# Kernel optimization log

Measured on AMD Instinct MI355X. Metric: run time of the kernel, lower is better.

The kernel has to match this reference:

```python
import jax, jax.numpy as jnp
import numpy as np

N_POS, D_MODEL, D_SAE, TOP_K = 2, 1024, 32768, 32


def setup_inputs() -> dict:
    key = jax.random.key(0)
    k_x, k_we, k_wd = jax.random.split(key, 3)
    x = jax.random.normal(k_x, (4096, N_POS, D_MODEL), dtype=jnp.float32)
    W_enc = jax.random.normal(k_we, (N_POS, D_MODEL, D_SAE), dtype=jnp.float32) * (1.0 / D_MODEL ** 0.5)
    W_dec = jax.random.normal(k_wd, (D_SAE, N_POS, D_MODEL), dtype=jnp.float32) * (1.0 / D_SAE ** 0.5)
    b_enc = jnp.zeros((D_SAE,), dtype=jnp.float32)
    b_dec = jnp.zeros((N_POS, D_MODEL), dtype=jnp.float32)
    return {"x": x, "W_enc": W_enc, "W_dec": W_dec, "b_enc": b_enc, "b_dec": b_dec}


def reference(x, W_enc, W_dec, b_enc, b_dec):
    # Encode: per-position einsum then shared bias -> (batch, d_sae)
    pre_act = jnp.einsum('btd,tds->bs', x, W_enc) + b_enc
    top_vals, top_idx = jax.lax.top_k(pre_act, TOP_K)  # (b, k)
    batch = pre_act.shape[0]
    rows = jnp.arange(batch)[:, None]  # (b, 1) broadcast against (b, k)
    z = jnp.zeros_like(pre_act).at[rows, top_idx].set(jax.nn.relu(top_vals))
    # Decode: dense contraction over d_sae -> (batch, n_positions, d_model)
    x_hat = jnp.einsum('bs,std->btd', z, W_dec) + b_dec
    return x_hat
```

## Files before the change

### kernel.cpp

```cpp
#include <hip/hip_runtime.h>
#include <cstdint>
#include <cstddef>

typedef unsigned short u16;
typedef unsigned long long u64;
typedef __attribute__((ext_vector_type(8))) short short8;
typedef __attribute__((ext_vector_type(4))) float f32x4;

constexpr int K_DIM = 2048;
constexpr int S_DIM = 32768;
constexpr int TOPK  = 32;
constexpr int CAP   = 256;
#define EPS      0.07f
#define THR_EMIT 3.7f
#define HIST_LO  3.5f

__device__ __forceinline__ u16 f2bf(float f) {
    unsigned u = __float_as_uint(f);
    return (u16)((u + 0x7FFFu + ((u >> 16) & 1u)) >> 16);
}
__device__ __forceinline__ float bf2f(u16 h) {
    return __uint_as_float(((unsigned)h) << 16);
}
__device__ __forceinline__ unsigned key_map(float f) {
    unsigned u = __float_as_uint(f);
    return (u & 0x80000000u) ? ~u : (u | 0x80000000u);
}
__device__ __forceinline__ float key_unmap(unsigned k) {
    unsigned u = (k & 0x80000000u) ? (k ^ 0x80000000u) : ~k;
    return __uint_as_float(u);
}

__global__ __launch_bounds__(256) void init_kernel(int* __restrict__ flag, int M)
{
    int i = blockIdx.x * 256 + threadIdx.x;
    if (i < M) flag[i] = 0;
}

__global__ __launch_bounds__(256) void conv_x_kernel(
    const float* __restrict__ x, u16* __restrict__ hi, int n4)
{
    int i = blockIdx.x * 256 + threadIdx.x;
    if (i >= n4) return;
    float4 v = ((const float4*)x)[i];
    ushort4 h;
    h.x = f2bf(v.x); h.y = f2bf(v.y); h.z = f2bf(v.z); h.w = f2bf(v.w);
    ((ushort4*)hi)[i] = h;
}

__global__ __launch_bounds__(256) void conv_wt_kernel(
    const float* __restrict__ W, float* __restrict__ WT, u16* __restrict__ Wh)
{
    __shared__ float tile[64][65];
    const int t  = threadIdx.x;
    const int s0 = blockIdx.x * 64;
    const int k0 = blockIdx.y * 64;
#pragma unroll
    for (int i = 0; i < 4; ++i) {
        int kl = (t >> 4) + i * 16;
        int sc = (t & 15) * 4;
        float4 v = *(const float4*)&W[(size_t)(k0 + kl) * S_DIM + s0 + sc];
        tile[kl][sc] = v.x; tile[kl][sc + 1] = v.y;
        tile[kl][sc + 2] = v.z; tile[kl][sc + 3] = v.w;
    }
    __syncthreads();
    const int klc = (t & 7) * 8;
#pragma unroll
    for (int i = 0; i < 2; ++i) {
        int sl = (t >> 3) + i * 32;
        float f[8];
        short8 h8;
#pragma unroll
        for (int j = 0; j < 8; ++j) {
            f[j] = tile[klc + j][sl];
            h8[j] = (short)f2bf(f[j]);
        }
        size_t o = (size_t)(s0 + sl) * K_DIM + k0 + klc;
        *(float4*)&WT[o]     = make_float4(f[0], f[1], f[2], f[3]);
        *(float4*)&WT[o + 4] = make_float4(f[4], f[5], f[6], f[7]);
        *(short8*)&Wh[o] = h8;
    }
}

__device__ __forceinline__ void gl16(const u16* g, u16* s) {
    __builtin_amdgcn_global_load_lds(
        (const __attribute__((address_space(1))) unsigned int*)g,
        (__attribute__((address_space(3))) unsigned int*)s,
        16, 0, 0);
}

#define LGKM0  do { asm volatile("s_waitcnt lgkmcnt(0)" ::: "memory"); \
                    __builtin_amdgcn_sched_barrier(0); } while (0)
#define VMW(n) asm volatile("s_waitcnt vmcnt(" #n ")" ::: "memory")
#define BAR    do { __builtin_amdgcn_s_barrier(); \
                    __builtin_amdgcn_sched_barrier(0); } while (0)

__global__ __launch_bounds__(512, 2) void gemm_mfma_kernel(
    const u16* __restrict__ A, const u16* __restrict__ B,
    const float* __restrict__ bias, u16* __restrict__ Cb)
{
    __shared__ alignas(16) u16 sMem[65536];
    u16* sA0 = sMem;
    u16* sB0 = sMem + 32768;

    const int t = threadIdx.x;
    const int lane = t & 63;
    const int w = t >> 6;
    const int wm = w >> 2, wn = w & 3;

    const int nwg = gridDim.x;
    const int q = nwg >> 3;
    const int bid = blockIdx.x;
    const int wg = (bid & 7) * q + (bid >> 3);
    const int bm = wg >> 7;
    const int bn = wg & 127;

    const u16* Ab = A + (size_t)bm * 256 * K_DIM;
    const u16* Bb = B + (size_t)bn * 256 * K_DIM;

    const int w2  = w * 2;
    const int lr3 = lane >> 3;
    const int csw = ((lane & 7) ^ lr3) * 8;

    const int rl = lane & 15, kq = lane >> 4;
    const int swz = rl & 7;
    const int ac0 = (kq ^ swz) * 8;
    const int ac1 = ((4 + kq) ^ swz) * 8;
    const int arow = (wm * 16 + rl) * 64;
    const int brow = (wn * 16 + rl) * 64;

    f32x4 acc[8][4];
#pragma unroll
    for (int m = 0; m < 8; ++m)
#pragma unroll
        for (int n = 0; n < 4; ++n) acc[m][n] = (f32x4){0.f, 0.f, 0.f, 0.f};

    auto stA = [&](int half, int j, int kt, int buf) {
        const u16* src = Ab + (size_t)(half * 128 + (w2 + j) * 8 + lr3) * K_DIM
                            + kt * 64 + csw;
        gl16(src, sA0 + buf * 16384 + half * 8192 + (w2 + j) * 512);
    };
    auto stB = [&](int half, int j, int kt, int buf) {
        const u16* src = Bb + (size_t)(half * 128 + (w2 + j) * 8 + lr3) * K_DIM
                            + kt * 64 + csw;
        gl16(src, sB0 + buf * 16384 + half * 8192 + (w2 + j) * 512);
    };

    stB(0, 0, 0, 0); stB(0, 1, 0, 0);
    stA(0, 0, 0, 0); stA(0, 1, 0, 0);
    stB(1, 0, 0, 0); stB(1, 1, 0, 0);
    stA(1, 0, 0, 0); stA(1, 1, 0, 0);
    stB(0, 0, 1, 1); stB(0, 1, 1, 1);
    stA(0, 0, 1, 1); stA(0, 1, 1, 1);
    stB(1, 0, 1, 1); stB(1, 1, 1, 1);
    VMW(6);
    BAR;

    short8 af[4][2], bf[4][2];

#pragma unroll
    for (int n = 0; n < 2; ++n) {
        bf[n][0] = *(const short8*)&sB0[brow + n * 4096 + ac0];
        bf[n][1] = *(const short8*)&sB0[brow + n * 4096 + ac1];
    }

#pragma unroll 1
    for (int it = 0; it < 16; ++it) {
        const bool lastIt = (it == 15);
#pragma unroll
        for (int h = 0; h < 2; ++h) {
            const int b  = h;
            const int tA = 2 * it + 1 + h;
            const int tB = 2 * it + 2 + h;

#pragma unroll
            for (int m = 0; m < 4; ++m) {
                af[m][0] = *(const short8*)&sA0[b * 16384 + arow + m * 2048 + ac0];
                af[m][1] = *(const short8*)&sA0[b * 16384 + arow + m * 2048 + ac1];
            }
            if (tA < 32) { stA(1, 0, tA, b ^ 1); stA(1, 1, tA, b ^ 1); }
            __builtin_amdgcn_s_barrier();
            LGKM0;
            __builtin_amdgcn_s_setprio(1);
#pragma unroll
            for (int m = 0; m < 4; ++m)
#pragma unroll
                for (int n = 0; n < 2; ++n)
#pragma unroll
                    for (int kk = 0; kk < 2; ++kk)
                        acc[m][n] = __builtin_amdgcn_mfma_f32_16x16x32_bf16(
                            af[m][kk], bf[n][kk], acc[m][n], 0, 0, 0);
            __builtin_amdgcn_s_setprio(0);
            BAR;

#pragma unroll
            for (int n = 2; n < 4; ++n) {
                bf[n][0] = *(const short8*)&sB0[b * 16384 + brow + n * 4096 + ac0];
                bf[n][1] = *(const short8*)&sB0[b * 16384 + brow + n * 4096 + ac1];
            }
            if (tB < 32) { stB(0, 0, tB, b); stB(0, 1, tB, b); }
            __builtin_amdgcn_s_barrier();
            LGKM0;
            __builtin_amdgcn_s_setprio(1);
#pragma unroll
            for (int m = 0; m < 4; ++m)
#pragma unroll
                for (int n = 2; n < 4; ++n)
#pragma unroll
                    for (int kk = 0; kk < 2; ++kk)
                        acc[m][n] = __builtin_amdgcn_mfma_f32_16x16x32_bf16(
                            af[m][kk], bf[n][kk], acc[m][n], 0, 0, 0);
            __builtin_amdgcn_s_setprio(0);
            BAR;

#pragma unroll
            for (int m = 0; m < 4; ++m) {
                af[m][0] = *(const short8*)&sA0[b * 16384 + arow + (m + 4) * 2048 + ac0];
                af[m][1] = *(const short8*)&sA0[b * 16384 + arow + (m + 4) * 2048 + ac1];
            }
            if (tB < 32) { stA(0, 0, tB, b); stA(0, 1, tB, b); }
            __builtin_amdgcn_s_barrier();
            LGKM0;
            __builtin_amdgcn_s_setprio(1);
#pragma unroll
            for (int m = 0; m < 4; ++m)
#pragma unroll
                for (int n = 2; n < 4; ++n)
#pragma unroll
                    for (int kk = 0; kk < 2; ++kk)
                        acc[m + 4][n] = __builtin_amdgcn_mfma_f32_16x16x32_bf16(
                            af[m][kk], bf[n][kk], acc[m + 4][n], 0, 0, 0);
            __builtin_amdgcn_s_setprio(0);
            BAR;

            if (tB < 32) { stB(1, 0, tB, b); stB(1, 1, tB, b); }
            __builtin_amdgcn_s_barrier();
            __builtin_amdgcn_s_setprio(1);
#pragma unroll
            for (int m = 0; m < 4; ++m)
#pragma unroll
                for (int n = 0; n < 2; ++n)
#pragma unroll
                    for (int kk = 0; kk < 2; ++kk)
                        acc[m + 4][n] = __builtin_amdgcn_mfma_f32_16x16x32_bf16(
                            af[m][kk], bf[n][kk], acc[m + 4][n], 0, 0, 0);
            __builtin_amdgcn_s_setprio(0);
            if (lastIt && h == 0) { VMW(0); } else { VMW(6); }
            if (!(lastIt && h == 1)) {
#pragma unroll
                for (int n = 0; n < 2; ++n) {
                    bf[n][0] = *(const short8*)&sB0[(b ^ 1) * 16384 + brow + n * 4096 + ac0];
                    bf[n][1] = *(const short8*)&sB0[(b ^ 1) * 16384 + brow + n * 4096 + ac1];
                }
            }
            BAR;
        }
    }

    {
        const int colL = wn * 16 + rl;
        const int rowL = wm * 16 + kq * 4;
        float bv[4];
#pragma unroll
        for (int n = 0; n < 4; ++n) bv[n] = bias[bn * 256 + colL + n * 64];
#pragma unroll
        for (int m = 0; m < 8; ++m)
#pragma unroll
            for (int n = 0; n < 4; ++n)
#pragma unroll
                for (int rr = 0; rr < 4; ++rr)
                    sMem[(rowL + m * 32 + rr) * 256 + colL + n * 64] =
                        f2bf(acc[m][n][rr] + bv[n]);
        __syncthreads();

        const int rr2 = t >> 5;
        const int c16 = t & 31;
        const size_t growB = (size_t)bm * 256;
#pragma unroll
        for (int r = 0; r < 16; ++r) {
            const int lrow = r * 16 + rr2;
            short8 v = *(const short8*)&sMem[lrow * 256 + c16 * 8];
            *(short8*)&Cb[(growB + lrow) * S_DIM + bn * 256 + c16 * 8] = v;
        }
    }
}

__global__ __launch_bounds__(256) void screen_kernel(
    const u16* __restrict__ pre, u64* __restrict__ emit,
    int* __restrict__ ccnt, float* __restrict__ thrv,
    int* __restrict__ flag, int row0)
{
    __shared__ unsigned hist[64];
    __shared__ int cnt;

    const int t = threadIdx.x;
    const int row = blockIdx.x;
    const int grow = row0 + row;
    const u16* prow = pre + (size_t)row * S_DIM;

    if (t < 64) hist[t] = 0;
    if (t == 0) cnt = 0;
    __syncthreads();

    u64* erow = emit + (size_t)grow * CAP;
    for (int i = t * 8; i < S_DIM; i += 2048) {
        short8 v8 = *(const short8*)&prow[i];
#pragma unroll
        for (int j = 0; j < 8; ++j) {
            float v = bf2f((u16)v8[j]);
            if (v >= HIST_LO) {
                int b = (int)((v - HIST_LO) * 25.0f);
                if (b > 63) b = 63;
                atomicAdd(&hist[b], 1u);
                if (v >= THR_EMIT) {
                    int p = atomicAdd(&cnt, 1);
                    if (p < CAP)
                        erow[p] = ((u64)key_map(v) << 32) | (unsigned)(i + j);
                }
            }
        }
    }
    __syncthreads();

    if (t == 0) {
        unsigned acc = 0;
        int b = -1;
        for (int j = 63; j >= 0; --j) {
            acc += hist[j];
            if (acc >= (unsigned)TOPK) { b = j; break; }
        }
        float thr = HIST_LO + 0.04f * b - 2.0f * EPS - 1e-4f;
        if (b < 0 || cnt > CAP || thr < THR_EMIT) {
            flag[grow] = 1;
            thr = THR_EMIT;
        }
        thrv[grow] = thr;
        ccnt[grow] = (cnt < CAP) ? cnt : CAP;
    }
}

__global__ __launch_bounds__(256) void rescore_kernel(
    const float* __restrict__ x, const float* __restrict__ WT,
    const float* __restrict__ benc, const u64* __restrict__ emit,
    const int* __restrict__ ccnt, const float* __restrict__ thrv,
    float* __restrict__ resc, int row0)
{
    const int row = row0 + blockIdx.x;
    const int t = threadIdx.x;
    const int w = t >> 6, l = t & 63;
    const int cnt = ccnt[row];
    const float thr = thrv[row];

    __shared__ float xs[K_DIM];
    const float* xr = x + (size_t)row * K_DIM;
    for (int i = t * 4; i < K_DIM; i += 1024)
        *(float4*)&xs[i] = *(const float4*)&xr[i];
    __syncthreads();

    for (int c = w; c < cnt; c += 4) {
        const u64 pk = emit[(size_t)row * CAP + c];
        const float approx = key_unmap((unsigned)(pk >> 32));
        if (approx < thr) {
            if (l == 0) resc[(size_t)row * CAP + c] = -3e38f;
            continue;
        }
        const int s = (int)(pk & 0xFFFFFFFFu);
        const float* wc = WT + (size_t)s * K_DIM;
        float acc = 0.f;
#pragma unroll
        for (int j = 0; j < 32; ++j)
            acc = fmaf(xs[l + 64 * j], wc[l + 64 * j], acc);
#pragma unroll
        for (int d = 1; d < 64; d <<= 1) acc += __shfl_xor(acc, d);
        if (l == 0) resc[(size_t)row * CAP + c] = acc + benc[s];
    }
}

__global__ __launch_bounds__(64) void select_kernel(
    const float* __restrict__ resc, const u64* __restrict__ emit,
    const int* __restrict__ ccnt, const float* __restrict__ thrv,
    float* __restrict__ tv, int* __restrict__ ti, int* __restrict__ flag,
    int row0)
{
    const int row = row0 + blockIdx.x;
    const int l = threadIdx.x;
    const int cnt = ccnt[row];

    float v[4] = {0.f, 0.f, 0.f, 0.f};
    int   s[4] = {-1, -1, -1, -1};
    u64   p[4] = {0, 0, 0, 0};
#pragma unroll
    for (int j = 0; j < 4; ++j) {
        int c = l + j * 64;
        if (c < cnt) {
            s[j] = (int)(emit[(size_t)row * CAP + c] & 0xFFFFFFFFu);
            v[j] = resc[(size_t)row * CAP + c];
            p[j] = ((u64)key_map(v[j]) << 32) | (unsigned)(~s[j]);
        }
    }

    float* tvr = tv + (size_t)row * TOPK;
    int*   tir = ti + (size_t)row * TOPK;
    float v32f = -3e38f;
#pragma unroll 1
    for (int r = 0; r < TOPK; ++r) {
        u64 m = p[0];
        if (p[1] > m) m = p[1];
        if (p[2] > m) m = p[2];
        if (p[3] > m) m = p[3];
#pragma unroll
        for (int d = 1; d < 64; d <<= 1) {
            u64 o = __shfl_xor(m, d);
            if (o > m) m = o;
        }
        if (r == TOPK - 1) v32f = key_unmap((unsigned)(m >> 32));
        if (p[0] == m)      { tvr[r] = v[0]; tir[r] = s[0] < 0 ? 0 : s[0]; p[0] = 0; }
        else if (p[1] == m) { tvr[r] = v[1]; tir[r] = s[1] < 0 ? 0 : s[1]; p[1] = 0; }
        else if (p[2] == m) { tvr[r] = v[2]; tir[r] = s[2] < 0 ? 0 : s[2]; p[2] = 0; }
        else if (p[3] == m) { tvr[r] = v[3]; tir[r] = s[3] < 0 ? 0 : s[3]; p[3] = 0; }
    }
    if (l == 0) {
        if (v32f < thrv[row] + EPS) flag[row] = 1;
    }
}

__global__ __launch_bounds__(256) void fb_screen_kernel(
    const u16* __restrict__ pre, u64* __restrict__ emit,
    int* __restrict__ ccnt, const int* __restrict__ flag, int row0)
{
    const int grow = row0 + blockIdx.x;
    if (!flag[grow]) return;

    __shared__ unsigned hist[2048];
    __shared__ unsigned partial[256];
    __shared__ unsigned sh_tk;
    __shared__ int cnt;

    const int t = threadIdx.x;
    const u16* prow = pre + (size_t)blockIdx.x * S_DIM;

    for (int i = t; i < 2048; i += 256) hist[i] = 0;
    if (t == 0) cnt = 0;
    __syncthreads();

    for (int i = t * 8; i < S_DIM; i += 2048) {
        short8 v8 = *(const short8*)&prow[i];
#pragma unroll
        for (int j = 0; j < 8; ++j) {
            unsigned k = key_map(bf2f((u16)v8[j]));
            if (k >= 0xC0000000u) atomicAdd(&hist[(k >> 19) - 6144], 1u);
        }
    }
    __syncthreads();

    unsigned ps = 0;
#pragma unroll
    for (int j = 0; j < 8; ++j) ps += hist[t * 8 + j];
    partial[t] = ps;
    __syncthreads();

    if (t == 0) {
        unsigned acc = 0;
        int seg = -1;
        for (int s = 255; s >= 0; --s) {
            if (acc + partial[s] >= (unsigned)TOPK) { seg = s; break; }
            acc += partial[s];
        }
        int bucket = 6144;
        if (seg >= 0) {
            for (int b = seg * 8 + 7; b >= seg * 8; --b) {
                acc += hist[b];
                if (acc >= (unsigned)TOPK) { bucket = 6144 + b; break; }
            }
        }
        float lo = key_unmap(((unsigned)bucket) << 19) - 2.0f * EPS;
        sh_tk = key_map(lo);
    }
    __syncthreads();

    const unsigned TK = sh_tk;
    u64* erow = emit + (size_t)grow * CAP;
    for (int i = t * 8; i < S_DIM; i += 2048) {
        short8 v8 = *(const short8*)&prow[i];
#pragma unroll
        for (int j = 0; j < 8; ++j) {
            unsigned k = key_map(bf2f((u16)v8[j]));
            if (k >= TK) {
                int p = atomicAdd(&cnt, 1);
                if (p < CAP) erow[p] = ((u64)k << 32) | (unsigned)(i + j);
            }
        }
    }
    __syncthreads();
    if (t == 0) ccnt[grow] = (cnt < CAP) ? cnt : CAP;
}

__global__ __launch_bounds__(256) void fb_rescore_kernel(
    const float* __restrict__ x, const float* __restrict__ WT,
    const float* __restrict__ benc, const u64* __restrict__ emit,
    const int* __restrict__ ccnt, float* __restrict__ resc,
    const int* __restrict__ flag, int row0)
{
    const int row = row0 + blockIdx.x;
    if (!flag[row]) return;
    const int t = threadIdx.x;
    const int w = t >> 6, l = t & 63;
    const int cnt = ccnt[row];

    __shared__ float xs[K_DIM];
    const float* xr = x + (size_t)row * K_DIM;
    for (int i = t * 4; i < K_DIM; i += 1024)
        *(float4*)&xs[i] = *(const float4*)&xr[i];
    __syncthreads();

    for (int c = w; c < cnt; c += 4) {
        const int s = (int)(emit[(size_t)row * CAP + c] & 0xFFFFFFFFu);
        const float* wc = WT + (size_t)s * K_DIM;
        float acc = 0.f;
#pragma unroll
        for (int j = 0; j < 32; ++j)
            acc = fmaf(xs[l + 64 * j], wc[l + 64 * j], acc);
#pragma unroll
        for (int d = 1; d < 64; d <<= 1) acc += __shfl_xor(acc, d);
        if (l == 0) resc[(size_t)row * CAP + c] = acc + benc[s];
    }
}

__global__ __launch_bounds__(64) void fb_select_kernel(
    const float* __restrict__ resc, const u64* __restrict__ emit,
    const int* __restrict__ ccnt, float* __restrict__ tv,
    int* __restrict__ ti, const int* __restrict__ flag, int row0)
{
    const int row = row0 + blockIdx.x;
    if (!flag[row]) return;
    const int l = threadIdx.x;
    const int cnt = ccnt[row];

    float v[4] = {0.f, 0.f, 0.f, 0.f};
    int   s[4] = {-1, -1, -1, -1};
    u64   p[4] = {0, 0, 0, 0};
#pragma unroll
    for (int j = 0; j < 4; ++j) {
        int c = l + j * 64;
        if (c < cnt) {
            s[j] = (int)(emit[(size_t)row * CAP + c] & 0xFFFFFFFFu);
            v[j] = resc[(size_t)row * CAP + c];
            p[j] = ((u64)key_map(v[j]) << 32) | (unsigned)(~s[j]);
        }
    }

    float* tvr = tv + (size_t)row * TOPK;
    int*   tir = ti + (size_t)row * TOPK;
#pragma unroll 1
    for (int r = 0; r < TOPK; ++r) {
        u64 m = p[0];
        if (p[1] > m) m = p[1];
        if (p[2] > m) m = p[2];
        if (p[3] > m) m = p[3];
#pragma unroll
        for (int d = 1; d < 64; d <<= 1) {
            u64 o = __shfl_xor(m, d);
            if (o > m) m = o;
        }
        if (p[0] == m)      { tvr[r] = v[0]; tir[r] = s[0] < 0 ? 0 : s[0]; p[0] = 0; }
        else if (p[1] == m) { tvr[r] = v[1]; tir[r] = s[1] < 0 ? 0 : s[1]; p[1] = 0; }
        else if (p[2] == m) { tvr[r] = v[2]; tir[r] = s[2] < 0 ? 0 : s[2]; p[2] = 0; }
        else if (p[3] == m) { tvr[r] = v[3]; tir[r] = s[3] < 0 ? 0 : s[3]; p[3] = 0; }
    }
}

__global__ __launch_bounds__(256) void decode_kernel(
    const float* __restrict__ tval, const int* __restrict__ tidx,
    const float* __restrict__ Wd, const float* __restrict__ bdec,
    float* __restrict__ out, int row0)
{
    const int row = row0 + blockIdx.x;
    const int t = threadIdx.x;
    __shared__ float sv[TOPK];
    __shared__ int   si[TOPK];
    if (t < TOPK) {
        sv[t] = fmaxf(tval[(size_t)row * TOPK + t], 0.f);
        si[t] = tidx[(size_t)row * TOPK + t];
    }
    __syncthreads();

    const int c0 = t * 4;
    float4 acc0 = *(const float4*)(bdec + c0);
    float4 acc1 = *(const float4*)(bdec + 1024 + c0);
#pragma unroll 4
    for (int i = 0; i < TOPK; ++i) {
        const float z = sv[i];
        if (z > 0.f) {
            const float* wr = Wd + (size_t)si[i] * K_DIM;
            float4 w0 = *(const float4*)(wr + c0);
            float4 w1 = *(const float4*)(wr + 1024 + c0);
            acc0.x = fmaf(z, w0.x, acc0.x); acc0.y = fmaf(z, w0.y, acc0.y);
            acc0.z = fmaf(z, w0.z, acc0.z); acc0.w = fmaf(z, w0.w, acc0.w);
            acc1.x = fmaf(z, w1.x, acc1.x); acc1.y = fmaf(z, w1.y, acc1.y);
            acc1.z = fmaf(z, w1.z, acc1.z); acc1.w = fmaf(z, w1.w, acc1.w);
        }
    }
    float* op = out + (size_t)row * K_DIM;
    *(float4*)(op + c0) = acc0;
    *(float4*)(op + 1024 + c0) = acc1;
}

extern "C" void kernel_launch(void* const* d_in, const int* in_sizes, int n_in,
                              void* d_out, int out_size, void* d_ws, size_t ws_size,
                              hipStream_t stream)
{
    const float* x     = (const float*)d_in[0];
    const float* W_enc = (const float*)d_in[1];
    const float* W_dec = (const float*)d_in[2];
    const float* b_enc = (const float*)d_in[3];
    const float* b_dec = (const float*)d_in[4];
    float* out = (float*)d_out;

    const int M = in_sizes[0] / K_DIM;

    char* wsb = (char*)d_ws;
    size_t o = 0;
    float*    tv   = (float*)(wsb + o);    o += (size_t)M * TOPK * 4;
    int*      ti   = (int*)(wsb + o);      o += (size_t)M * TOPK * 4;
    u64*      emit = (u64*)(wsb + o);      o += (size_t)M * CAP * 8;
    int*      ccnt = (int*)(wsb + o);      o += (size_t)M * 4;
    float*    thrv = (float*)(wsb + o);    o += (size_t)M * 4;
    int*      flag = (int*)(wsb + o);      o += (size_t)M * 4;
    float*    resc = (float*)(wsb + o);    o += (size_t)M * CAP * 4;
    u16*      Xh   = (u16*)(wsb + o);      o += (size_t)M * K_DIM * 2;
    u16*      Wh   = (u16*)(wsb + o);      o += (size_t)S_DIM * K_DIM * 2;
    float*    WT   = (float*)(wsb + o);    o += (size_t)S_DIM * K_DIM * 4;
    u16*      pre  = (u16*)(wsb + o);

    size_t cap = (ws_size > o) ? (ws_size - o) : 0;
    long cap_rows = (long)(cap / ((size_t)S_DIM * 2));
    int chunk = (int)((cap_rows / 256) * 256);
    if (chunk <= 0) chunk = 256;
    if (chunk > M) chunk = M;

    init_kernel<<<(M + 255) / 256, 256, 0, stream>>>(flag, M);
    const int n4 = M * K_DIM / 4;
    conv_x_kernel<<<(n4 + 255) / 256, 256, 0, stream>>>(x, Xh, n4);
    conv_wt_kernel<<<dim3(S_DIM / 64, K_DIM / 64), 256, 0, stream>>>(W_enc, WT, Wh);

    for (int r0 = 0; r0 < M; r0 += chunk) {
        const int rows = (M - r0 < chunk) ? (M - r0) : chunk;
        const int nbm = rows / 256;
        gemm_mfma_kernel<<<nbm * 128, 512, 0, stream>>>(
            Xh + (size_t)r0 * K_DIM, Wh, b_enc, pre);
        screen_kernel<<<rows, 256, 0, stream>>>(pre, emit, ccnt, thrv, flag, r0);
        rescore_kernel<<<rows, 256, 0, stream>>>(x, WT, b_enc, emit, ccnt, thrv, resc, r0);
        select_kernel<<<rows, 64, 0, stream>>>(resc, emit, ccnt, thrv, tv, ti, flag, r0);
        fb_screen_kernel<<<rows, 256, 0, stream>>>(pre, emit, ccnt, flag, r0);
        fb_rescore_kernel<<<rows, 256, 0, stream>>>(x, WT, b_enc, emit, ccnt, resc, flag, r0);
        fb_select_kernel<<<rows, 64, 0, stream>>>(resc, emit, ccnt, tv, ti, flag, r0);
        decode_kernel<<<rows, 256, 0, stream>>>(tv, ti, W_dec, b_dec, out, r0);
    }
}
```

Before: 1.084 ms.

## Fuse screen/rescore/select/decode into one per-row kernel and swizzle GEMM epilogue LDS

Merges the screen, rescore, select and decode kernels into a single per-row kernel that keeps candidates, rescored values and top-k results in shared memory. The fallback path is merged the same way and overwrites the output for flagged rows. This removes several launches and the global-memory round-trips for emit, resc, tv and ti, and drops the flag init kernel. Separately, the GEMM epilogue's shared-memory tile gets an XOR swizzle to cut bank conflicts. Per-block LDS use grows, which may lower occupancy in the fused kernels.

```diff
diff --git a/kernel.cpp b/kernel.cpp
--- a/kernel.cpp
+++ b/kernel.cpp
@@ -29,12 +29,6 @@
 __device__ __forceinline__ float key_unmap(unsigned k) {
     unsigned u = (k & 0x80000000u) ? (k ^ 0x80000000u) : ~k;
     return __uint_as_float(u);
-}
-
-__global__ __launch_bounds__(256) void init_kernel(int* __restrict__ flag, int M)
-{
-    int i = blockIdx.x * 256 + threadIdx.x;
-    if (i < M) flag[i] = 0;
 }
 
 __global__ __launch_bounds__(256) void conv_x_kernel(
@@ -268,9 +262,13 @@
 #pragma unroll
             for (int n = 0; n < 4; ++n)
 #pragma unroll
-                for (int rr = 0; rr < 4; ++rr)
-                    sMem[(rowL + m * 32 + rr) * 256 + colL + n * 64] =
+                for (int rr = 0; rr < 4; ++rr) {
+                    const int row = rowL + m * 32 + rr;
+                    const int col = colL + n * 64;
+                    const int chs = (col >> 3) ^ (((row >> 2) & 3) << 1);
+                    sMem[row * 256 + (chs << 3) + (col & 7)] =
                         f2bf(acc[m][n][rr] + bv[n]);
+                }
         __syncthreads();
 
         const int rr2 = t >> 5;
@@ -279,19 +277,28 @@
 #pragma unroll
         for (int r = 0; r < 16; ++r) {
             const int lrow = r * 16 + rr2;
-            short8 v = *(const short8*)&sMem[lrow * 256 + c16 * 8];
+            const int chr = c16 ^ (((lrow >> 2) & 3) << 1);
+            short8 v = *(const short8*)&sMem[lrow * 256 + (chr << 3)];
             *(short8*)&Cb[(growB + lrow) * S_DIM + bn * 256 + c16 * 8] = v;
         }
     }
 }
 
-__global__ __launch_bounds__(256) void screen_kernel(
-    const u16* __restrict__ pre, u64* __restrict__ emit,
-    int* __restrict__ ccnt, float* __restrict__ thrv,
-    int* __restrict__ flag, int row0)
+__global__ __launch_bounds__(256) void fused_kernel(
+    const u16* __restrict__ pre, const float* __restrict__ x,
+    const float* __restrict__ WT, const float* __restrict__ benc,
+    const float* __restrict__ Wd, const float* __restrict__ bdec,
+    float* __restrict__ out, int* __restrict__ flag, int row0)
 {
     __shared__ unsigned hist[64];
     __shared__ int cnt;
+    __shared__ float sh_thr;
+    __shared__ int sh_bad;
+    __shared__ u64 emitL[CAP];
+    __shared__ float rescL[CAP];
+    __shared__ float xs[K_DIM];
+    __shared__ float tvL[TOPK];
+    __shared__ int   tiL[TOPK];
 
     const int t = threadIdx.x;
     const int row = blockIdx.x;
@@ -299,10 +306,13 @@
     const u16* prow = pre + (size_t)row * S_DIM;
 
     if (t < 64) hist[t] = 0;
-    if (t == 0) cnt = 0;
-    __syncthreads();
-
-    u64* erow = emit + (size_t)grow * CAP;
+    if (t == 0) { cnt = 0; sh_bad = 0; }
+    __syncthreads();
+
+    const float* xr = x + (size_t)grow * K_DIM;
+    for (int i = t * 4; i < K_DIM; i += 1024)
+        *(float4*)&xs[i] = *(const float4*)&xr[i];
+
     for (int i = t * 8; i < S_DIM; i += 2048) {
         short8 v8 = *(const short8*)&prow[i];
 #pragma unroll
@@ -315,7 +325,7 @@
                 if (v >= THR_EMIT) {
                     int p = atomicAdd(&cnt, 1);
                     if (p < CAP)
-                        erow[p] = ((u64)key_map(v) << 32) | (unsigned)(i + j);
+                        emitL[p] = ((u64)key_map(v) << 32) | (unsigned)(i + j);
                 }
             }
         }
@@ -331,37 +341,22 @@
         }
         float thr = HIST_LO + 0.04f * b - 2.0f * EPS - 1e-4f;
         if (b < 0 || cnt > CAP || thr < THR_EMIT) {
-            flag[grow] = 1;
+            sh_bad = 1;
             thr = THR_EMIT;
         }
-        thrv[grow] = thr;
-        ccnt[grow] = (cnt < CAP) ? cnt : CAP;
-    }
-}
-
-__global__ __launch_bounds__(256) void rescore_kernel(
-    const float* __restrict__ x, const float* __restrict__ WT,
-    const float* __restrict__ benc, const u64* __restrict__ emit,
-    const int* __restrict__ ccnt, const float* __restrict__ thrv,
-    float* __restrict__ resc, int row0)
-{
-    const int row = row0 + blockIdx.x;
-    const int t = threadIdx.x;
-    const int w = t >> 6, l = t & 63;
-    const int cnt = ccnt[row];
-    const float thr = thrv[row];
-
-    __shared__ float xs[K_DIM];
-    const float* xr = x + (size_t)row * K_DIM;
-    for (int i = t * 4; i < K_DIM; i += 1024)
-        *(float4*)&xs[i] = *(const float4*)&xr[i];
-    __syncthreads();
-
-    for (int c = w; c < cnt; c += 4) {
-        const u64 pk = emit[(size_t)row * CAP + c];
+        sh_thr = thr;
+    }
+    __syncthreads();
+
+    const int cntc = (cnt < CAP) ? cnt : CAP;
+    const float thr = sh_thr;
+    const int wv = t >> 6, l = t & 63;
+
+    for (int c = wv; c < cntc; c += 4) {
+        const u64 pk = emitL[c];
         const float approx = key_unmap((unsigned)(pk >> 32));
         if (approx < thr) {
-            if (l == 0) resc[(size_t)row * CAP + c] = -3e38f;
+            if (l == 0) rescL[c] = -3e38f;
             continue;
         }
         const int s = (int)(pk & 0xFFFFFFFFu);
@@ -372,76 +367,97 @@
             acc = fmaf(xs[l + 64 * j], wc[l + 64 * j], acc);
 #pragma unroll
         for (int d = 1; d < 64; d <<= 1) acc += __shfl_xor(acc, d);
-        if (l == 0) resc[(size_t)row * CAP + c] = acc + benc[s];
-    }
-}
-
-__global__ __launch_bounds__(64) void select_kernel(
-    const float* __restrict__ resc, const u64* __restrict__ emit,
-    const int* __restrict__ ccnt, const float* __restrict__ thrv,
-    float* __restrict__ tv, int* __restrict__ ti, int* __restrict__ flag,
-    int row0)
+        if (l == 0) rescL[c] = acc + benc[s];
+    }
+    __syncthreads();
+
+    if (t < 64) {
+        float v[4] = {0.f, 0.f, 0.f, 0.f};
+        int   s[4] = {-1, -1, -1, -1};
+        u64   p[4] = {0, 0, 0, 0};
+#pragma unroll
+        for (int j = 0; j < 4; ++j) {
+            int c = l + j * 64;
+            if (c < cntc) {
+                s[j] = (int)(emitL[c] & 0xFFFFFFFFu);
+                v[j] = rescL[c];
+                p[j] = ((u64)key_map(v[j]) << 32) | (unsigned)(~s[j]);
+            }
+        }
+        float v32f = -3e38f;
+#pragma unroll 1
+        for (int r = 0; r < TOPK; ++r) {
+            u64 m = p[0];
+            if (p[1] > m) m = p[1];
+            if (p[2] > m) m = p[2];
+            if (p[3] > m) m = p[3];
+#pragma unroll
+            for (int d = 1; d < 64; d <<= 1) {
+                u64 o = __shfl_xor(m, d);
+                if (o > m) m = o;
+            }
+            if (r == TOPK - 1) v32f = key_unmap((unsigned)(m >> 32));
+            if (p[0] == m)      { tvL[r] = v[0]; tiL[r] = s[0] < 0 ? 0 : s[0]; p[0] = 0; }
+            else if (p[1] == m) { tvL[r] = v[1]; tiL[r] = s[1] < 0 ? 0 : s[1]; p[1] = 0; }
+            else if (p[2] == m) { tvL[r] = v[2]; tiL[r] = s[2] < 0 ? 0 : s[2]; p[2] = 0; }
+            else if (p[3] == m) { tvL[r] = v[3]; tiL[r] = s[3] < 0 ? 0 : s[3]; p[3] = 0; }
+        }
+        if (l == 0)
+            flag[grow] = (sh_bad || v32f < thr + EPS) ? 1 : 0;
+    }
+    __syncthreads();
+
+    const int c0 = t * 4;
+    float4 acc0 = *(const float4*)(bdec + c0);
+    float4 acc1 = *(const float4*)(bdec + 1024 + c0);
+#pragma unroll 4
+    for (int i = 0; i < TOPK; ++i) {
+        const float z = fmaxf(tvL[i], 0.f);
+        if (z > 0.f) {
+            const float* wr = Wd + (size_t)tiL[i] * K_DIM;
+            float4 w0 = *(const float4*)(wr + c0);
+            float4 w1 = *(const float4*)(wr + 1024 + c0);
+            acc0.x = fmaf(z, w0.x, acc0.x); acc0.y = fmaf(z, w0.y, acc0.y);
+            acc0.z = fmaf(z, w0.z, acc0.z); acc0.w = fmaf(z, w0.w, acc0.w);
+            acc1.x = fmaf(z, w1.x, acc1.x); acc1.y = fmaf(z, w1.y, acc1.y);
+            acc1.z = fmaf(z, w1.z, acc1.z); acc1.w = fmaf(z, w1.w, acc1.w);
+        }
+    }
+    float* op = out + (size_t)grow * K_DIM;
+    *(float4*)(op + c0) = acc0;
+    *(float4*)(op + 1024 + c0) = acc1;
+}
+
+__global__ __launch_bounds__(256) void fb_kernel(
+    const u16* __restrict__ pre, const float* __restrict__ x,
+    const float* __restrict__ WT, const float* __restrict__ benc,
+    const float* __restrict__ Wd, const float* __restrict__ bdec,
+    float* __restrict__ out, const int* __restrict__ flag, int row0)
 {
-    const int row = row0 + blockIdx.x;
-    const int l = threadIdx.x;
-    const int cnt = ccnt[row];
-
-    float v[4] = {0.f, 0.f, 0.f, 0.f};
-    int   s[4] = {-1, -1, -1, -1};
-    u64   p[4] = {0, 0, 0, 0};
-#pragma unroll
-    for (int j = 0; j < 4; ++j) {
-        int c = l + j * 64;
-        if (c < cnt) {
-            s[j] = (int)(emit[(size_t)row * CAP + c] & 0xFFFFFFFFu);
-            v[j] = resc[(size_t)row * CAP + c];
-            p[j] = ((u64)key_map(v[j]) << 32) | (unsigned)(~s[j]);
-        }
-    }
-
-    float* tvr = tv + (size_t)row * TOPK;
-    int*   tir = ti + (size_t)row * TOPK;
-    float v32f = -3e38f;
-#pragma unroll 1
-    for (int r = 0; r < TOPK; ++r) {
-        u64 m = p[0];
-        if (p[1] > m) m = p[1];
-        if (p[2] > m) m = p[2];
-        if (p[3] > m) m = p[3];
-#pragma unroll
-        for (int d = 1; d < 64; d <<= 1) {
-            u64 o = __shfl_xor(m, d);
-            if (o > m) m = o;
-        }
-        if (r == TOPK - 1) v32f = key_unmap((unsigned)(m >> 32));
-        if (p[0] == m)      { tvr[r] = v[0]; tir[r] = s[0] < 0 ? 0 : s[0]; p[0] = 0; }
-        else if (p[1] == m) { tvr[r] = v[1]; tir[r] = s[1] < 0 ? 0 : s[1]; p[1] = 0; }
-        else if (p[2] == m) { tvr[r] = v[2]; tir[r] = s[2] < 0 ? 0 : s[2]; p[2] = 0; }
-        else if (p[3] == m) { tvr[r] = v[3]; tir[r] = s[3] < 0 ? 0 : s[3]; p[3] = 0; }
-    }
-    if (l == 0) {
-        if (v32f < thrv[row] + EPS) flag[row] = 1;
-    }
-}
-
-__global__ __launch_bounds__(256) void fb_screen_kernel(
-    const u16* __restrict__ pre, u64* __restrict__ emit,
-    int* __restrict__ ccnt, const int* __restrict__ flag, int row0)
-{
-    const int grow = row0 + blockIdx.x;
+    const int row = blockIdx.x;
+    const int grow = row0 + row;
     if (!flag[grow]) return;
 
     __shared__ unsigned hist[2048];
     __shared__ unsigned partial[256];
     __shared__ unsigned sh_tk;
     __shared__ int cnt;
+    __shared__ u64 emitL[CAP];
+    __shared__ float rescL[CAP];
+    __shared__ float xs[K_DIM];
+    __shared__ float tvL[TOPK];
+    __shared__ int   tiL[TOPK];
 
     const int t = threadIdx.x;
-    const u16* prow = pre + (size_t)blockIdx.x * S_DIM;
+    const u16* prow = pre + (size_t)row * S_DIM;
 
     for (int i = t; i < 2048; i += 256) hist[i] = 0;
     if (t == 0) cnt = 0;
     __syncthreads();
+
+    const float* xr = x + (size_t)grow * K_DIM;
+    for (int i = t * 4; i < K_DIM; i += 1024)
+        *(float4*)&xs[i] = *(const float4*)&xr[i];
 
     for (int i = t * 8; i < S_DIM; i += 2048) {
         short8 v8 = *(const short8*)&prow[i];
@@ -479,7 +495,6 @@
     __syncthreads();
 
     const unsigned TK = sh_tk;
-    u64* erow = emit + (size_t)grow * CAP;
     for (int i = t * 8; i < S_DIM; i += 2048) {
         short8 v8 = *(const short8*)&prow[i];
 #pragma unroll
@@ -487,34 +502,17 @@
             unsigned k = key_map(bf2f((u16)v8[j]));
             if (k >= TK) {
                 int p = atomicAdd(&cnt, 1);
-                if (p < CAP) erow[p] = ((u64)k << 32) | (unsigned)(i + j);
-            }
-        }
-    }
-    __syncthreads();
-    if (t == 0) ccnt[grow] = (cnt < CAP) ? cnt : CAP;
-}
-
-__global__ __launch_bounds__(256) void fb_rescore_kernel(
-    const float* __restrict__ x, const float* __restrict__ WT,
-    const float* __restrict__ benc, const u64* __restrict__ emit,
-    const int* __restrict__ ccnt, float* __restrict__ resc,
-    const int* __restrict__ flag, int row0)
-{
-    const int row = row0 + blockIdx.x;
-    if (!flag[row]) return;
-    const int t = threadIdx.x;
-    const int w = t >> 6, l = t & 63;
-    const int cnt = ccnt[row];
-
-    __shared__ float xs[K_DIM];
-    const float* xr = x + (size_t)row * K_DIM;
-    for (int i = t * 4; i < K_DIM; i += 1024)
-        *(float4*)&xs[i] = *(const float4*)&xr[i];
-    __syncthreads();
-
-    for (int c = w; c < cnt; c += 4) {
-        const int s = (int)(emit[(size_t)row * CAP + c] & 0xFFFFFFFFu);
+                if (p < CAP) emitL[p] = ((u64)k << 32) | (unsigned)(i + j);
+            }
+        }
+    }
+    __syncthreads();
+
+    const int cntc = (cnt < CAP) ? cnt : CAP;
+    const int wv = t >> 6, l = t & 63;
+
+    for (int c = wv; c < cntc; c += 4) {
+        const int s = (int)(emitL[c] & 0xFFFFFFFFu);
         const float* wc = WT + (size_t)s * K_DIM;
         float acc = 0.f;
 #pragma unroll
@@ -522,65 +520,39 @@
             acc = fmaf(xs[l + 64 * j], wc[l + 64 * j], acc);
 #pragma unroll
         for (int d = 1; d < 64; d <<= 1) acc += __shfl_xor(acc, d);
-        if (l == 0) resc[(size_t)row * CAP + c] = acc + benc[s];
-    }
-}
-
-__global__ __launch_bounds__(64) void fb_select_kernel(
-    const float* __restrict__ resc, const u64* __restrict__ emit,
-    const int* __restrict__ ccnt, float* __restrict__ tv,
-    int* __restrict__ ti, const int* __restrict__ flag, int row0)
-{
-    const int row = row0 + blockIdx.x;
-    if (!flag[row]) return;
-    const int l = threadIdx.x;
-    const int cnt = ccnt[row];
-
-    float v[4] = {0.f, 0.f, 0.f, 0.f};
-    int   s[4] = {-1, -1, -1, -1};
-    u64   p[4] = {0, 0, 0, 0};
-#pragma unroll
-    for (int j = 0; j < 4; ++j) {
-        int c = l + j * 64;
-        if (c < cnt) {
-            s[j] = (int)(emit[(size_t)row * CAP + c] & 0xFFFFFFFFu);
-            v[j] = resc[(size_t)row * CAP + c];
-            p[j] = ((u64)key_map(v[j]) << 32) | (unsigned)(~s[j]);
-        }
-    }
-
-    float* tvr = tv + (size_t)row * TOPK;
-    int*   tir = ti + (size_t)row * TOPK;
+        if (l == 0) rescL[c] = acc + benc[s];
+    }
+    __syncthreads();
+
+    if (t < 64) {
+        float v[4] = {0.f, 0.f, 0.f, 0.f};
+        int   s[4] = {-1, -1, -1, -1};
+        u64   p[4] = {0, 0, 0, 0};
+#pragma unroll
+        for (int j = 0; j < 4; ++j) {
+            int c = l + j * 64;
+            if (c < cntc) {
+                s[j] = (int)(emitL[c] & 0xFFFFFFFFu);
+                v[j] = rescL[c];
+                p[j] = ((u64)key_map(v[j]) << 32) | (unsigned)(~s[j]);
+            }
+        }
 #pragma unroll 1
-    for (int r = 0; r < TOPK; ++r) {
-        u64 m = p[0];
-        if (p[1] > m) m = p[1];
-        if (p[2] > m) m = p[2];
-        if (p[3] > m) m = p[3];
-#pragma unroll
-        for (int d = 1; d < 64; d <<= 1) {
-            u64 o = __shfl_xor(m, d);
-            if (o > m) m = o;
-        }
-        if (p[0] == m)      { tvr[r] = v[0]; tir[r] = s[0] < 0 ? 0 : s[0]; p[0] = 0; }
-        else if (p[1] == m) { tvr[r] = v[1]; tir[r] = s[1] < 0 ? 0 : s[1]; p[1] = 0; }
-        else if (p[2] == m) { tvr[r] = v[2]; tir[r] = s[2] < 0 ? 0 : s[2]; p[2] = 0; }
-        else if (p[3] == m) { tvr[r] = v[3]; tir[r] = s[3] < 0 ? 0 : s[3]; p[3] = 0; }
-    }
-}
-
-__global__ __launch_bounds__(256) void decode_kernel(
-    const float* __restrict__ tval, const int* __restrict__ tidx,
-    const float* __restrict__ Wd, const float* __restrict__ bdec,
-    float* __restrict__ out, int row0)
-{
-    const int row = row0 + blockIdx.x;
-    const int t = threadIdx.x;
-    __shared__ float sv[TOPK];
-    __shared__ int   si[TOPK];
-    if (t < TOPK) {
-        sv[t] = fmaxf(tval[(size_t)row * TOPK + t], 0.f);
-        si[t] = tidx[(size_t)row * TOPK + t];
+        for (int r = 0; r < TOPK; ++r) {
+            u64 m = p[0];
+            if (p[1] > m) m = p[1];
+            if (p[2] > m) m = p[2];
+            if (p[3] > m) m = p[3];
+#pragma unroll
+            for (int d = 1; d < 64; d <<= 1) {
+                u64 o = __shfl_xor(m, d);
+                if (o > m) m = o;
+            }
+            if (p[0] == m)      { tvL[r] = v[0]; tiL[r] = s[0] < 0 ? 0 : s[0]; p[0] = 0; }
+            else if (p[1] == m) { tvL[r] = v[1]; tiL[r] = s[1] < 0 ? 0 : s[1]; p[1] = 0; }
+            else if (p[2] == m) { tvL[r] = v[2]; tiL[r] = s[2] < 0 ? 0 : s[2]; p[2] = 0; }
+            else if (p[3] == m) { tvL[r] = v[3]; tiL[r] = s[3] < 0 ? 0 : s[3]; p[3] = 0; }
+        }
     }
     __syncthreads();
 
@@ -589,9 +561,9 @@
     float4 acc1 = *(const float4*)(bdec + 1024 + c0);
 #pragma unroll 4
     for (int i = 0; i < TOPK; ++i) {
-        const float z = sv[i];
+        const float z = fmaxf(tvL[i], 0.f);
         if (z > 0.f) {
-            const float* wr = Wd + (size_t)si[i] * K_DIM;
+            const float* wr = Wd + (size_t)tiL[i] * K_DIM;
             float4 w0 = *(const float4*)(wr + c0);
             float4 w1 = *(const float4*)(wr + 1024 + c0);
             acc0.x = fmaf(z, w0.x, acc0.x); acc0.y = fmaf(z, w0.y, acc0.y);
@@ -600,7 +572,7 @@
             acc1.z = fmaf(z, w1.z, acc1.z); acc1.w = fmaf(z, w1.w, acc1.w);
         }
     }
-    float* op = out + (size_t)row * K_DIM;
+    float* op = out + (size_t)grow * K_DIM;
     *(float4*)(op + c0) = acc0;
     *(float4*)(op + 1024 + c0) = acc1;
 }
@@ -620,17 +592,11 @@
 
     char* wsb = (char*)d_ws;
     size_t o = 0;
-    float*    tv   = (float*)(wsb + o);    o += (size_t)M * TOPK * 4;
-    int*      ti   = (int*)(wsb + o);      o += (size_t)M * TOPK * 4;
-    u64*      emit = (u64*)(wsb + o);      o += (size_t)M * CAP * 8;
-    int*      ccnt = (int*)(wsb + o);      o += (size_t)M * 4;
-    float*    thrv = (float*)(wsb + o);    o += (size_t)M * 4;
-    int*      flag = (int*)(wsb + o);      o += (size_t)M * 4;
-    float*    resc = (float*)(wsb + o);    o += (size_t)M * CAP * 4;
-    u16*      Xh   = (u16*)(wsb + o);      o += (size_t)M * K_DIM * 2;
-    u16*      Wh   = (u16*)(wsb + o);      o += (size_t)S_DIM * K_DIM * 2;
-    float*    WT   = (float*)(wsb + o);    o += (size_t)S_DIM * K_DIM * 4;
-    u16*      pre  = (u16*)(wsb + o);
+    int*   flag = (int*)(wsb + o);   o += (size_t)M * 4;
+    u16*   Xh   = (u16*)(wsb + o);   o += (size_t)M * K_DIM * 2;
+    u16*   Wh   = (u16*)(wsb + o);   o += (size_t)S_DIM * K_DIM * 2;
+    float* WT   = (float*)(wsb + o); o += (size_t)S_DIM * K_DIM * 4;
+    u16*   pre  = (u16*)(wsb + o);
 
     size_t cap = (ws_size > o) ? (ws_size - o) : 0;
     long cap_rows = (long)(cap / ((size_t)S_DIM * 2));
@@ -638,7 +604,6 @@
     if (chunk <= 0) chunk = 256;
     if (chunk > M) chunk = M;
 
-    init_kernel<<<(M + 255) / 256, 256, 0, stream>>>(flag, M);
     const int n4 = M * K_DIM / 4;
     conv_x_kernel<<<(n4 + 255) / 256, 256, 0, stream>>>(x, Xh, n4);
     conv_wt_kernel<<<dim3(S_DIM / 64, K_DIM / 64), 256, 0, stream>>>(W_enc, WT, Wh);
@@ -648,12 +613,9 @@
         const int nbm = rows / 256;
         gemm_mfma_kernel<<<nbm * 128, 512, 0, stream>>>(
             Xh + (size_t)r0 * K_DIM, Wh, b_enc, pre);
-        screen_kernel<<<rows, 256, 0, stream>>>(pre, emit, ccnt, thrv, flag, r0);
-        rescore_kernel<<<rows, 256, 0, stream>>>(x, WT, b_enc, emit, ccnt, thrv, resc, r0);
-        select_kernel<<<rows, 64, 0, stream>>>(resc, emit, ccnt, thrv, tv, ti, flag, r0);
-        fb_screen_kernel<<<rows, 256, 0, stream>>>(pre, emit, ccnt, flag, r0);
-        fb_rescore_kernel<<<rows, 256, 0, stream>>>(x, WT, b_enc, emit, ccnt, resc, flag, r0);
-        fb_select_kernel<<<rows, 64, 0, stream>>>(resc, emit, ccnt, tv, ti, flag, r0);
-        decode_kernel<<<rows, 256, 0, stream>>>(tv, ti, W_dec, b_dec, out, r0);
-    }
-}
+        fused_kernel<<<rows, 256, 0, stream>>>(
+            pre, x, WT, b_enc, W_dec, b_dec, out, flag, r0);
+        fb_kernel<<<rows, 256, 0, stream>>>(
+            pre, x, WT, b_enc, W_dec, b_dec, out, flag, r0);
+    }
+}
```

Measured after the change: 1.070 ms. No clear change (-1.3%).
